# Kernel tuning notes

Measured on AMD Instinct MI355X. Metric: run time of the kernel, lower is better.

The kernel has to match this reference:

```python
import jax, jax.numpy as jnp
import numpy as np

B, S, D, H, R, P = 4, 8192, 512, 8, 64, 4
HD = D // H  # 64
EPS = 1e-6


def _sketch_p4(z, G1, G2):
    # sketchwithnegativity(z, 2): M1 = M2 = z
    inv_sqrt_r = 1.0 / np.sqrt(R).astype(np.float32)
    half = inv_sqrt_r * ((z @ G1) * (z @ G2))  # [B,H,S,R]
    return half * half  # sketch(): half * half for p=4


def setup_inputs() -> dict:
    key = jax.random.key(0)
    ks = jax.random.split(key, 16)
    lin = lambda k: jax.random.normal(k, (D, D), jnp.float32) * (1.0 / np.sqrt(D))
    g = lambda k: jax.random.normal(k, (HD, R), jnp.float32) * (1.0 / np.sqrt(R))
    return {
        "x": jax.random.normal(ks[0], (B, S, D), jnp.float32),
        "Wq": lin(ks[1]), "bq": jnp.zeros((D,), jnp.float32),
        "Wk": lin(ks[2]), "bk": jnp.zeros((D,), jnp.float32),
        "Wv": lin(ks[3]), "bv": jnp.zeros((D,), jnp.float32),
        "Wp": lin(ks[4]), "bp": jnp.zeros((D,), jnp.float32),
        "gamma_q": jnp.ones((1,), jnp.float32), "beta_q": jnp.zeros((1,), jnp.float32),
        "gamma_k": jnp.ones((1,), jnp.float32), "beta_k": jnp.zeros((1,), jnp.float32),
        "qG1": g(ks[5]), "qG2": g(ks[6]),
        "kG1": g(ks[7]), "kG2": g(ks[8]),
    }


def reference(x, Wq, bq, Wk, bk, Wv, bv, Wp, bp,
              gamma_q, beta_q, gamma_k, beta_k, qG1, qG2, kG1, kG2):
    b, s, d = x.shape
    split = lambda t: t.reshape(b, s, H, HD).transpose(0, 2, 1, 3)  # [B,H,S,HD]
    q = split(x @ Wq + bq)
    k = split(x @ Wk + bk)
    v = split(x @ Wv + bv)
    q = gamma_q * q + beta_q
    k = gamma_k * k + beta_k
    phi_q = _sketch_p4(q, qG1, qG2)  # [B,H,S,R]
    phi_k = _sketch_p4(k, kG1, kG2)  # [B,H,S,R]
    # linear-attention form of attn = (phi_q phi_k^T) / rowsum; avoids [S,S]
    kv = jnp.einsum('bhsr,bhsd->bhrd', phi_k, v)          # [B,H,R,HD]
    ksum = phi_k.sum(axis=2)                              # [B,H,R]
    num = jnp.einsum('bhqr,bhrd->bhqd', phi_q, kv)        # [B,H,S,HD]
    den = jnp.einsum('bhqr,bhr->bhq', phi_q, ksum) + EPS  # [B,H,S]
    out = num / den[..., None]
    out = out.transpose(0, 2, 1, 3).reshape(b, s, d)
    return out @ Wp + bp
```

## Files before the change

kernel.cpp:

```cpp
#include <hip/hip_runtime.h>
#include <hip/hip_bf16.h>


#define SEQ 8192

typedef __attribute__((ext_vector_type(8))) short bf16x8;
typedef __attribute__((ext_vector_type(4))) float f32x4;

__device__ __forceinline__ unsigned short f2b(float f) {
    union { float f; unsigned int i; } v; v.f = f;
    unsigned int r = v.i + 0x7fffu + ((v.i >> 16) & 1u);
    return (unsigned short)(r >> 16);
}
__device__ __forceinline__ float b2f(unsigned short u) {
    union { unsigned int i; float f; } v; v.i = ((unsigned int)u) << 16; return v.f;
}

#if __has_builtin(__builtin_amdgcn_global_load_lds)
#define ASYNC_CP 1
#endif

__device__ __forceinline__ void cp16(const unsigned short* g, unsigned short* l) {
#ifdef ASYNC_CP
    __builtin_amdgcn_global_load_lds(
        (const __attribute__((address_space(1))) unsigned int*)g,
        (__attribute__((address_space(3))) unsigned int*)l, 16, 0, 0);
#endif
}

__global__ __launch_bounds__(256) void convert_x(
    const float* __restrict__ x, unsigned short* __restrict__ xb)
{
    size_t i = ((size_t)blockIdx.x * 256 + threadIdx.x) * 8;
    float4 a = *(const float4*)&x[i];
    float4 b = *(const float4*)&x[i + 4];
    ushort4 o1 = { f2b(a.x), f2b(a.y), f2b(a.z), f2b(a.w) };
    ushort4 o2 = { f2b(b.x), f2b(b.y), f2b(b.z), f2b(b.w) };
    *(ushort4*)&xb[i]     = o1;
    *(ushort4*)&xb[i + 4] = o2;
}

__global__ __launch_bounds__(256) void convert_wT(
    const float* __restrict__ Wv, const float* __restrict__ Wp,
    unsigned short* __restrict__ WTf, unsigned short* __restrict__ WTp)
{
    const int z = blockIdx.z;
    const float* W = (z == 0) ? Wv : Wp;
    unsigned short* O = (z == 0) ? (WTf + (size_t)2048 * 512) : WTp;
    __shared__ float t[32][33];
    const int tid = threadIdx.x;
    const int tx = tid & 31, ty = tid >> 5;
    const int k0 = blockIdx.x * 32, n0 = blockIdx.y * 32;
    #pragma unroll
    for (int i = 0; i < 4; ++i)
        t[ty + 8 * i][tx] = W[(size_t)(k0 + ty + 8 * i) * 512 + n0 + tx];
    __syncthreads();
    #pragma unroll
    for (int i = 0; i < 4; ++i)
        O[(size_t)(n0 + ty + 8 * i) * 512 + k0 + tx] = f2b(t[tx][ty + 8 * i]);
}

__global__ __launch_bounds__(256) void precompute_wc(
    const float* __restrict__ Wq, const float* __restrict__ bq,
    const float* __restrict__ Wk, const float* __restrict__ bk,
    const float* __restrict__ bv,
    const float* __restrict__ gq, const float* __restrict__ bbq,
    const float* __restrict__ gk, const float* __restrict__ bbk,
    const float* __restrict__ qG1, const float* __restrict__ qG2,
    const float* __restrict__ kG1, const float* __restrict__ kG2,
    unsigned short* __restrict__ WTf, float* __restrict__ cvec)
{
    const int bi = blockIdx.x;
    const int tid = threadIdx.x;
    if (bi == 32) {
        if (blockIdx.y == 0)
            for (int i = tid; i < 512; i += 256) cvec[2048 + i] = bv[i];
        return;
    }
    const int zz = bi >> 4, h = (bi >> 1) & 7, p = bi & 1;
    const float* W    = zz ? Wk : Wq;
    const float* bias = zz ? bk : bq;
    const float* G    = zz ? (p ? kG2 : kG1) : (p ? qG2 : qG1);
    const float  gamma = zz ? gk[0] : gq[0];
    const float  beta  = zz ? bbk[0] : bbq[0];

    __shared__ float Gs[64][65];
    for (int i = tid; i < 4096; i += 256) Gs[i >> 6][i & 63] = G[i];
    __syncthreads();

    const int rr = tid & 63, kg = tid >> 6;
    const int jc = zz * 1024 + h * 128 + rr * 2 + p;
    const int k0 = blockIdx.y * 32;
    for (int k = k0 + kg; k < k0 + 32; k += 4) {
        float s = 0.f;
        const float* wrow = &W[(size_t)k * 512 + h * 64];
        #pragma unroll 8
        for (int j = 0; j < 64; ++j) s = fmaf(wrow[j], Gs[j][rr], s);
        WTf[(size_t)jc * 512 + k] = f2b(gamma * s);
    }
    if (kg == 0 && blockIdx.y == 0) {
        float cb = 0.f, cg = 0.f;
        #pragma unroll 8
        for (int j = 0; j < 64; ++j) {
            cb = fmaf(bias[h * 64 + j], Gs[j][rr], cb);
            cg += Gs[j][rr];
        }
        cvec[jc] = gamma * cb + beta * cg;
    }
}

__global__ __launch_bounds__(256) void gemm_mfma_fused(
    const unsigned short* __restrict__ xb,
    const unsigned short* __restrict__ WTf,
    const float* __restrict__ cvec,
    unsigned short* __restrict__ PHIQ, unsigned short* __restrict__ PHIKT,
    unsigned short* __restrict__ VT)
{
    __shared__ __align__(16) unsigned short As[128 * 32];
    __shared__ __align__(16) unsigned short Bs[128 * 32];
    __shared__ __align__(16) unsigned short ep[9216];

    const int tid = threadIdx.x;
    const int w = tid >> 6, lane = tid & 63;
    const int n0 = blockIdx.x * 128;
    const int j0 = blockIdx.y * 128;
    const int wr = w >> 1, wc = w & 1;

    const int r0 = w * 32 + (lane >> 2);
    const int kq = (((lane & 3) ^ ((lane >> 2) & 3)) * 8);
    const unsigned short* gA = &xb[(size_t)(n0 + r0) * 512 + kq];
    const unsigned short* gB = &WTf[(size_t)(j0 + r0) * 512 + kq];
    unsigned short* lA = &As[(w * 32) * 32];
    unsigned short* lB = &Bs[(w * 32) * 32];

    f32x4 acc[4][4];
    #pragma unroll
    for (int i = 0; i < 4; ++i)
        #pragma unroll
        for (int j = 0; j < 4; ++j) { acc[i][j] = (f32x4){0.f, 0.f, 0.f, 0.f}; }

    const int cr = (((lane >> 4) ^ (lane & 3)) * 8);

    for (int k0 = 0; k0 < 512; k0 += 32) {
        __syncthreads();
#ifdef ASYNC_CP
        cp16(gA + k0, lA);
        cp16(gA + 16 * 512 + k0, lA + 16 * 32);
        cp16(gB + k0, lB);
        cp16(gB + 16 * 512 + k0, lB + 16 * 32);
#else
        { uint4 v = *(const uint4*)(gA + k0);            *(uint4*)(lA + (size_t)lane * 8) = v; }
        { uint4 v = *(const uint4*)(gA + 16 * 512 + k0); *(uint4*)(lA + 16 * 32 + (size_t)lane * 8) = v; }
        { uint4 v = *(const uint4*)(gB + k0);            *(uint4*)(lB + (size_t)lane * 8) = v; }
        { uint4 v = *(const uint4*)(gB + 16 * 512 + k0); *(uint4*)(lB + 16 * 32 + (size_t)lane * 8) = v; }
#endif
        __syncthreads();

        bf16x8 af[4], bfr[4];
        #pragma unroll
        for (int i = 0; i < 4; ++i) {
            af[i]  = *(const bf16x8*)&As[(wr * 64 + i * 16 + (lane & 15)) * 32 + cr];
            bfr[i] = *(const bf16x8*)&Bs[(wc * 64 + i * 16 + (lane & 15)) * 32 + cr];
        }
        #pragma unroll
        for (int mi = 0; mi < 4; ++mi)
            #pragma unroll
            for (int ni = 0; ni < 4; ++ni)
                acc[mi][ni] = __builtin_amdgcn_mfma_f32_16x16x32_bf16(
                    af[mi], bfr[ni], acc[mi][ni], 0, 0, 0);
    }

    const int bq = n0 >> 13;
    const int sq = n0 & (SEQ - 1);

    if (j0 < 1024) {
        const int h = j0 >> 7;
        #pragma unroll
        for (int ni = 0; ni < 4; ++ni) {
            const int loc = wc * 64 + ni * 16 + (lane & 15);
            const float cv = cvec[j0 + loc];
            const int rr = loc >> 1;
            #pragma unroll
            for (int mi = 0; mi < 4; ++mi)
                #pragma unroll
                for (int r = 0; r < 4; ++r) {
                    float u = acc[mi][ni][r] + cv;
                    float up = __shfl_xor(u, 1);
                    float hh = 0.125f * u * up;
                    float phi = hh * hh;
                    if ((lane & 1) == 0)
                        ep[(wr * 64 + mi * 16 + (lane >> 4) * 4 + r) * 72 + rr] = f2b(phi);
                }
        }
        __syncthreads();
        for (int i = tid; i < 1024; i += 256) {
            const int tok = i >> 3, ch = i & 7;
            *(uint4*)&PHIQ[((size_t)(bq * 8 + h) * SEQ + sq + tok) * 64 + ch * 8] =
                *(const uint4*)&ep[tok * 72 + ch * 8];
        }
    } else if (j0 < 2048) {
        const int h = (j0 >> 7) & 7;
        #pragma unroll
        for (int ni = 0; ni < 4; ++ni) {
            const int loc = wc * 64 + ni * 16 + (lane & 15);
            const float cv = cvec[j0 + loc];
            const int rr = loc >> 1;
            #pragma unroll
            for (int mi = 0; mi < 4; ++mi)
                #pragma unroll
                for (int r = 0; r < 4; ++r) {
                    float u = acc[mi][ni][r] + cv;
                    float up = __shfl_xor(u, 1);
                    float hh = 0.125f * u * up;
                    float phi = hh * hh;
                    if ((lane & 1) == 0)
                        ep[rr * 136 + wr * 64 + mi * 16 + (lane >> 4) * 4 + r] = f2b(phi);
                }
        }
        __syncthreads();
        for (int i = tid; i < 1024; i += 256) {
            const int row = i >> 4, ch = i & 15;
            *(uint4*)&PHIKT[((size_t)((bq * 8 + h) * 64 + row)) * SEQ + sq + ch * 8] =
                *(const uint4*)&ep[row * 136 + ch * 8];
        }
    } else {
        #pragma unroll
        for (int half = 0; half < 2; ++half) {
            if (wc == half) {
                #pragma unroll
                for (int ni = 0; ni < 4; ++ni) {
                    const int loc = ni * 16 + (lane & 15);
                    const float cv = cvec[j0 + half * 64 + loc];
                    #pragma unroll
                    for (int mi = 0; mi < 4; ++mi)
                        #pragma unroll
                        for (int r = 0; r < 4; ++r)
                            ep[loc * 136 + wr * 64 + mi * 16 + (lane >> 4) * 4 + r] =
                                f2b(acc[mi][ni][r] + cv);
                }
            }
            __syncthreads();
            for (int i = tid; i < 1024; i += 256) {
                const int row = i >> 4, ch = i & 15;
                const int n = (j0 - 2048) + half * 64 + row;
                *(uint4*)&VT[((size_t)(bq * 512 + n)) * SEQ + sq + ch * 8] =
                    *(const uint4*)&ep[row * 136 + ch * 8];
            }
            __syncthreads();
        }
    }
}

__global__ __launch_bounds__(256) void gemm_mfma_final(
    const unsigned short* __restrict__ Ab,
    const unsigned short* __restrict__ WTp,
    const float* __restrict__ bias, float* __restrict__ out)
{
    __shared__ __align__(16) unsigned short As[128 * 32];
    __shared__ __align__(16) unsigned short Bs[128 * 32];

    const int tid = threadIdx.x;
    const int w = tid >> 6, lane = tid & 63;
    const int n0 = blockIdx.x * 128;
    const int j0 = blockIdx.y * 128;
    const int wr = w >> 1, wc = w & 1;

    const int r0 = w * 32 + (lane >> 2);
    const int kq = (((lane & 3) ^ ((lane >> 2) & 3)) * 8);
    const unsigned short* gA = &Ab[(size_t)(n0 + r0) * 512 + kq];
    const unsigned short* gB = &WTp[(size_t)(j0 + r0) * 512 + kq];
    unsigned short* lA = &As[(w * 32) * 32];
    unsigned short* lB = &Bs[(w * 32) * 32];

    f32x4 acc[4][4];
    #pragma unroll
    for (int i = 0; i < 4; ++i)
        #pragma unroll
        for (int j = 0; j < 4; ++j) { acc[i][j] = (f32x4){0.f, 0.f, 0.f, 0.f}; }

    const int cr = (((lane >> 4) ^ (lane & 3)) * 8);

    for (int k0 = 0; k0 < 512; k0 += 32) {
        __syncthreads();
#ifdef ASYNC_CP
        cp16(gA + k0, lA);
        cp16(gA + 16 * 512 + k0, lA + 16 * 32);
        cp16(gB + k0, lB);
        cp16(gB + 16 * 512 + k0, lB + 16 * 32);
#else
        { uint4 v = *(const uint4*)(gA + k0);            *(uint4*)(lA + (size_t)lane * 8) = v; }
        { uint4 v = *(const uint4*)(gA + 16 * 512 + k0); *(uint4*)(lA + 16 * 32 + (size_t)lane * 8) = v; }
        { uint4 v = *(const uint4*)(gB + k0);            *(uint4*)(lB + (size_t)lane * 8) = v; }
        { uint4 v = *(const uint4*)(gB + 16 * 512 + k0); *(uint4*)(lB + 16 * 32 + (size_t)lane * 8) = v; }
#endif
        __syncthreads();

        bf16x8 af[4], bfr[4];
        #pragma unroll
        for (int i = 0; i < 4; ++i) {
            af[i]  = *(const bf16x8*)&As[(wr * 64 + i * 16 + (lane & 15)) * 32 + cr];
            bfr[i] = *(const bf16x8*)&Bs[(wc * 64 + i * 16 + (lane & 15)) * 32 + cr];
        }
        #pragma unroll
        for (int mi = 0; mi < 4; ++mi)
            #pragma unroll
            for (int ni = 0; ni < 4; ++ni)
                acc[mi][ni] = __builtin_amdgcn_mfma_f32_16x16x32_bf16(
                    af[mi], bfr[ni], acc[mi][ni], 0, 0, 0);
    }

    #pragma unroll
    for (int ni = 0; ni < 4; ++ni) {
        const int jcol = j0 + wc * 64 + ni * 16 + (lane & 15);
        const float bvv = bias[jcol];
        #pragma unroll
        for (int mi = 0; mi < 4; ++mi) {
            #pragma unroll
            for (int r = 0; r < 4; ++r) {
                const int t = n0 + wr * 64 + mi * 16 + (lane >> 4) * 4 + r;
                out[(size_t)t * 512 + jcol] = acc[mi][ni][r] + bvv;
            }
        }
    }
}

__global__ __launch_bounds__(256) void kv_mfma(
    const unsigned short* __restrict__ PHIKT, const unsigned short* __restrict__ VT,
    float* __restrict__ KVP, float* __restrict__ KSP)
{
    const int bh = blockIdx.x, seg = blockIdx.y;
    const int tid = threadIdx.x;
    const int w = tid >> 6, lane = tid & 63;
    const size_t pbase =
        ((size_t)bh * 64 + w * 16 + (lane & 15)) * SEQ + seg * 256 + (lane >> 4) * 8;
    const size_t vbase =
        ((size_t)((bh >> 3) * 512 + (bh & 7) * 64 + (lane & 15))) * SEQ
        + seg * 256 + (lane >> 4) * 8;

    f32x4 acc[4], ks;
    #pragma unroll
    for (int nt = 0; nt < 4; ++nt) acc[nt] = (f32x4){0.f, 0.f, 0.f, 0.f};
    ks = (f32x4){0.f, 0.f, 0.f, 0.f};
    bf16x8 ones;
    #pragma unroll
    for (int i = 0; i < 8; ++i) ones[i] = (short)0x3f80;

    #pragma unroll 2
    for (int k = 0; k < 256; k += 32) {
        bf16x8 a = *(const bf16x8*)&PHIKT[pbase + k];
        ks = __builtin_amdgcn_mfma_f32_16x16x32_bf16(a, ones, ks, 0, 0, 0);
        #pragma unroll
        for (int nt = 0; nt < 4; ++nt) {
            bf16x8 bb = *(const bf16x8*)&VT[vbase + (size_t)nt * 16 * SEQ + k];
            acc[nt] = __builtin_amdgcn_mfma_f32_16x16x32_bf16(a, bb, acc[nt], 0, 0, 0);
        }
    }

    float* kvp = &KVP[((size_t)bh * 32 + seg) * 4096];
    #pragma unroll
    for (int nt = 0; nt < 4; ++nt) {
        float4 o = { acc[nt][0], acc[nt][1], acc[nt][2], acc[nt][3] };
        *(float4*)&kvp[(nt * 16 + (lane & 15)) * 64 + w * 16 + (lane >> 4) * 4] = o;
    }
    if ((lane & 15) == 0) {
        float4 o = { ks[0], ks[1], ks[2], ks[3] };
        *(float4*)&KSP[((size_t)bh * 32 + seg) * 64 + w * 16 + (lane >> 4) * 4] = o;
    }
}

__global__ __launch_bounds__(256) void kv_reduce(
    const float* __restrict__ KVP, const float* __restrict__ KSP,
    float* __restrict__ KV, float* __restrict__ KS)
{
    const int bh = blockIdx.x;
    const int e0 = blockIdx.y * 512;
    for (int e = e0 + threadIdx.x; e < e0 + 512; e += 256) {
        float s = 0.f;
        #pragma unroll 8
        for (int c = 0; c < 32; ++c) s += KVP[(size_t)(bh * 32 + c) * 4096 + e];
        KV[(size_t)bh * 4096 + e] = s;
    }
    if (blockIdx.y == 0 && threadIdx.x < 64) {
        float s = 0.f;
        for (int c = 0; c < 32; ++c) s += KSP[(bh * 32 + c) * 64 + threadIdx.x];
        KS[bh * 64 + threadIdx.x] = s;
    }
}

__global__ __launch_bounds__(256) void attn_mfma(
    const unsigned short* __restrict__ PHIQ, const float* __restrict__ KV,
    const float* __restrict__ KS, unsigned short* __restrict__ OAb)
{
    __shared__ __align__(16) unsigned short bpad[144 * 72];
    const int bh = blockIdx.x, st = blockIdx.y;
    const int tid = threadIdx.x;
    const int b = bh >> 3, h = bh & 7;

    for (int i = tid; i < 144 * 64; i += 256) {
        const int n = i >> 6, r = i & 63;
        float val;
        if (n < 64)        val = KV[(size_t)bh * 4096 + n * 64 + r];
        else if (n < 128)  { float x = KV[(size_t)bh * 4096 + (n - 64) * 64 + r];
                             val = x - b2f(f2b(x)); }
        else if (n == 128) val = KS[bh * 64 + r];
        else if (n == 129) { float x = KS[bh * 64 + r]; val = x - b2f(f2b(x)); }
        else               val = 0.f;
        bpad[n * 72 + r] = f2b(val);
    }
    __syncthreads();

    const int w = tid >> 6, lane = tid & 63;
    bf16x8 bf[9][2];
    #pragma unroll
    for (int nt = 0; nt < 9; ++nt) {
        const unsigned short* bp = &bpad[(nt * 16 + (lane & 15)) * 72 + (lane >> 4) * 8];
        bf[nt][0] = *(const bf16x8*)bp;
        bf[nt][1] = *(const bf16x8*)(bp + 32);
    }

    const int tw = st * 256 + w * 64;
    #pragma unroll
    for (int mt = 0; mt < 4; ++mt) {
        const unsigned short* ap =
            &PHIQ[((size_t)bh * SEQ + tw + mt * 16 + (lane & 15)) * 64 + (lane >> 4) * 8];
        bf16x8 a0 = *(const bf16x8*)ap;
        bf16x8 a1 = *(const bf16x8*)(ap + 32);
        f32x4 acc[9];
        #pragma unroll
        for (int nt = 0; nt < 9; ++nt) acc[nt] = (f32x4){0.f, 0.f, 0.f, 0.f};
        #pragma unroll
        for (int nt = 0; nt < 9; ++nt) {
            acc[nt] = __builtin_amdgcn_mfma_f32_16x16x32_bf16(a0, bf[nt][0], acc[nt], 0, 0, 0);
            acc[nt] = __builtin_amdgcn_mfma_f32_16x16x32_bf16(a1, bf[nt][1], acc[nt], 0, 0, 0);
        }
        #pragma unroll
        for (int r4 = 0; r4 < 4; ++r4) {
            const float den = __shfl(acc[8][r4], (lane & 48)) +
                              __shfl(acc[8][r4], (lane & 48) + 1) + 1e-6f;
            const float inv = 1.0f / den;
            const int s = tw + mt * 16 + (lane >> 4) * 4 + r4;
            #pragma unroll
            for (int nt = 0; nt < 4; ++nt)
                OAb[((size_t)b * SEQ + s) * 512 + h * 64 + nt * 16 + (lane & 15)] =
                    f2b((acc[nt][r4] + acc[nt + 4][r4]) * inv);
        }
    }
}

extern "C" void kernel_launch(void* const* d_in, const int* in_sizes, int n_in,
                              void* d_out, int out_size, void* d_ws, size_t ws_size,
                              hipStream_t stream)
{
    (void)in_sizes; (void)n_in; (void)out_size; (void)ws_size;
    const float* x   = (const float*)d_in[0];
    const float* Wq  = (const float*)d_in[1];
    const float* bq  = (const float*)d_in[2];
    const float* Wk  = (const float*)d_in[3];
    const float* bk  = (const float*)d_in[4];
    const float* Wv  = (const float*)d_in[5];
    const float* bv  = (const float*)d_in[6];
    const float* Wp  = (const float*)d_in[7];
    const float* bp  = (const float*)d_in[8];
    const float* gq  = (const float*)d_in[9];
    const float* bbq = (const float*)d_in[10];
    const float* gk  = (const float*)d_in[11];
    const float* bbk = (const float*)d_in[12];
    const float* qG1 = (const float*)d_in[13];
    const float* qG2 = (const float*)d_in[14];
    const float* kG1 = (const float*)d_in[15];
    const float* kG2 = (const float*)d_in[16];

    unsigned short* PHIQ  = (unsigned short*)d_ws;
    unsigned short* PHIKT = PHIQ + 16777216;
    unsigned short* VT    = PHIKT + 16777216;
    unsigned short* xb    = VT   + 16777216;
    unsigned short* OAb   = xb   + 16777216;
    unsigned short* WTf   = OAb  + 16777216;
    unsigned short* WTp   = WTf  + 2560 * 512;
    float* cvec = (float*)(WTp + 262144);
    float* KVP  = cvec + 2560;
    float* KSP  = KVP + 4194304;
    float* KV   = KSP + 65536;
    float* KS   = KV + 131072;
    float* out  = (float*)d_out;

    hipLaunchKernelGGL(convert_x, dim3(8192), dim3(256), 0, stream, x, xb);
    hipLaunchKernelGGL(convert_wT, dim3(16, 16, 2), dim3(256), 0, stream,
                       Wv, Wp, WTf, WTp);
    hipLaunchKernelGGL(precompute_wc, dim3(33, 16), dim3(256), 0, stream,
                       Wq, bq, Wk, bk, bv, gq, bbq, gk, bbk,
                       qG1, qG2, kG1, kG2, WTf, cvec);
    hipLaunchKernelGGL(gemm_mfma_fused, dim3(256, 20), dim3(256), 0, stream,
                       xb, WTf, cvec, PHIQ, PHIKT, VT);
    hipLaunchKernelGGL(kv_mfma, dim3(32, 32), dim3(256), 0, stream,
                       PHIKT, VT, KVP, KSP);
    hipLaunchKernelGGL(kv_reduce, dim3(32, 8), dim3(256), 0, stream, KVP, KSP, KV, KS);
    hipLaunchKernelGGL(attn_mfma, dim3(32, 32), dim3(256), 0, stream,
                       PHIQ, KV, KS, OAb);
    hipLaunchKernelGGL(gemm_mfma_final, dim3(256, 4), dim3(256), 0, stream,
                       OAb, WTp, bp, out);
}
```

Before: 417.0 us.

## Merge prep kernels, swap GEMM grid order, alias LDS, drop swizzle, halve KV segments

Folds the three preprocessing kernels into one prep_all launch that dispatches on block index, removing two launches. The two GEMM kernels swap grid axes so blocks sharing an x row tile launch next to each other, which should improve L2 reuse of the A operand. The fused GEMM aliases the epilogue buffer onto the A/B staging LDS to cut shared memory per block, guarded by an added barrier. The XOR swizzle on LDS loads is removed, which may reintroduce bank conflicts. kv_mfma now processes 512-length segments with 16 partials instead of 32, halving partial writes and reduce work but also halving parallelism.

```diff
diff --git a/kernel.cpp b/kernel.cpp
--- a/kernel.cpp
+++ b/kernel.cpp
@@ -28,39 +28,10 @@
 #endif
 }
 
-__global__ __launch_bounds__(256) void convert_x(
-    const float* __restrict__ x, unsigned short* __restrict__ xb)
-{
-    size_t i = ((size_t)blockIdx.x * 256 + threadIdx.x) * 8;
-    float4 a = *(const float4*)&x[i];
-    float4 b = *(const float4*)&x[i + 4];
-    ushort4 o1 = { f2b(a.x), f2b(a.y), f2b(a.z), f2b(a.w) };
-    ushort4 o2 = { f2b(b.x), f2b(b.y), f2b(b.z), f2b(b.w) };
-    *(ushort4*)&xb[i]     = o1;
-    *(ushort4*)&xb[i + 4] = o2;
-}
-
-__global__ __launch_bounds__(256) void convert_wT(
+__global__ __launch_bounds__(256) void prep_all(
+    const float* __restrict__ x, unsigned short* __restrict__ xb,
     const float* __restrict__ Wv, const float* __restrict__ Wp,
-    unsigned short* __restrict__ WTf, unsigned short* __restrict__ WTp)
-{
-    const int z = blockIdx.z;
-    const float* W = (z == 0) ? Wv : Wp;
-    unsigned short* O = (z == 0) ? (WTf + (size_t)2048 * 512) : WTp;
-    __shared__ float t[32][33];
-    const int tid = threadIdx.x;
-    const int tx = tid & 31, ty = tid >> 5;
-    const int k0 = blockIdx.x * 32, n0 = blockIdx.y * 32;
-    #pragma unroll
-    for (int i = 0; i < 4; ++i)
-        t[ty + 8 * i][tx] = W[(size_t)(k0 + ty + 8 * i) * 512 + n0 + tx];
-    __syncthreads();
-    #pragma unroll
-    for (int i = 0; i < 4; ++i)
-        O[(size_t)(n0 + ty + 8 * i) * 512 + k0 + tx] = f2b(t[tx][ty + 8 * i]);
-}
-
-__global__ __launch_bounds__(256) void precompute_wc(
+    unsigned short* __restrict__ WTf, unsigned short* __restrict__ WTp,
     const float* __restrict__ Wq, const float* __restrict__ bq,
     const float* __restrict__ Wk, const float* __restrict__ bk,
     const float* __restrict__ bv,
@@ -68,15 +39,46 @@
     const float* __restrict__ gk, const float* __restrict__ bbk,
     const float* __restrict__ qG1, const float* __restrict__ qG2,
     const float* __restrict__ kG1, const float* __restrict__ kG2,
-    unsigned short* __restrict__ WTf, float* __restrict__ cvec)
-{
-    const int bi = blockIdx.x;
+    float* __restrict__ cvec)
+{
+    const int blk = blockIdx.x;
     const int tid = threadIdx.x;
-    if (bi == 32) {
-        if (blockIdx.y == 0)
-            for (int i = tid; i < 512; i += 256) cvec[2048 + i] = bv[i];
+
+    if (blk < 8192) {
+        size_t i = ((size_t)blk * 256 + tid) * 8;
+        float4 a = *(const float4*)&x[i];
+        float4 b = *(const float4*)&x[i + 4];
+        ushort4 o1 = { f2b(a.x), f2b(a.y), f2b(a.z), f2b(a.w) };
+        ushort4 o2 = { f2b(b.x), f2b(b.y), f2b(b.z), f2b(b.w) };
+        *(ushort4*)&xb[i]     = o1;
+        *(ushort4*)&xb[i + 4] = o2;
         return;
     }
+
+    if (blk < 8704) {
+        const int idx = blk - 8192;
+        const int z = idx >> 8;
+        const float* W = (z == 0) ? Wv : Wp;
+        unsigned short* O = (z == 0) ? (WTf + (size_t)2048 * 512) : WTp;
+        __shared__ float t[32][33];
+        const int tx = tid & 31, ty = tid >> 5;
+        const int k0 = ((idx >> 4) & 15) * 32, n0 = (idx & 15) * 32;
+        #pragma unroll
+        for (int i = 0; i < 4; ++i)
+            t[ty + 8 * i][tx] = W[(size_t)(k0 + ty + 8 * i) * 512 + n0 + tx];
+        __syncthreads();
+        #pragma unroll
+        for (int i = 0; i < 4; ++i)
+            O[(size_t)(n0 + ty + 8 * i) * 512 + k0 + tx] = f2b(t[tx][ty + 8 * i]);
+        return;
+    }
+
+    const int idx = blk - 8704;
+    if (idx == 512) {
+        for (int i = tid; i < 512; i += 256) cvec[2048 + i] = bv[i];
+        return;
+    }
+    const int bi = idx & 31, ky = idx >> 5;
     const int zz = bi >> 4, h = (bi >> 1) & 7, p = bi & 1;
     const float* W    = zz ? Wk : Wq;
     const float* bias = zz ? bk : bq;
@@ -90,7 +92,7 @@
 
     const int rr = tid & 63, kg = tid >> 6;
     const int jc = zz * 1024 + h * 128 + rr * 2 + p;
-    const int k0 = blockIdx.y * 32;
+    const int k0 = ky * 32;
     for (int k = k0 + kg; k < k0 + 32; k += 4) {
         float s = 0.f;
         const float* wrow = &W[(size_t)k * 512 + h * 64];
@@ -98,7 +100,7 @@
         for (int j = 0; j < 64; ++j) s = fmaf(wrow[j], Gs[j][rr], s);
         WTf[(size_t)jc * 512 + k] = f2b(gamma * s);
     }
-    if (kg == 0 && blockIdx.y == 0) {
+    if (kg == 0 && ky == 0) {
         float cb = 0.f, cg = 0.f;
         #pragma unroll 8
         for (int j = 0; j < 64; ++j) {
@@ -116,22 +118,23 @@
     unsigned short* __restrict__ PHIQ, unsigned short* __restrict__ PHIKT,
     unsigned short* __restrict__ VT)
 {
-    __shared__ __align__(16) unsigned short As[128 * 32];
-    __shared__ __align__(16) unsigned short Bs[128 * 32];
-    __shared__ __align__(16) unsigned short ep[9216];
+    __shared__ __align__(16) unsigned short smem[9216];
+    unsigned short* As = smem;
+    unsigned short* Bs = smem + 4096;
+    unsigned short* ep = smem;
 
     const int tid = threadIdx.x;
     const int w = tid >> 6, lane = tid & 63;
-    const int n0 = blockIdx.x * 128;
-    const int j0 = blockIdx.y * 128;
+    const int j0 = blockIdx.x * 128;
+    const int n0 = blockIdx.y * 128;
     const int wr = w >> 1, wc = w & 1;
 
     const int r0 = w * 32 + (lane >> 2);
-    const int kq = (((lane & 3) ^ ((lane >> 2) & 3)) * 8);
+    const int kq = (lane & 3) * 8;
     const unsigned short* gA = &xb[(size_t)(n0 + r0) * 512 + kq];
     const unsigned short* gB = &WTf[(size_t)(j0 + r0) * 512 + kq];
-    unsigned short* lA = &As[(w * 32) * 32];
-    unsigned short* lB = &Bs[(w * 32) * 32];
+    unsigned short* lA = As + (w * 32) * 32;
+    unsigned short* lB = Bs + (w * 32) * 32;
 
     f32x4 acc[4][4];
     #pragma unroll
@@ -139,7 +142,7 @@
         #pragma unroll
         for (int j = 0; j < 4; ++j) { acc[i][j] = (f32x4){0.f, 0.f, 0.f, 0.f}; }
 
-    const int cr = (((lane >> 4) ^ (lane & 3)) * 8);
+    const int cr = (lane >> 4) * 8;
 
     for (int k0 = 0; k0 < 512; k0 += 32) {
         __syncthreads();
@@ -170,6 +173,7 @@
                     af[mi], bfr[ni], acc[mi][ni], 0, 0, 0);
     }
 
+    __syncthreads();
     const int bq = n0 >> 13;
     const int sq = n0 & (SEQ - 1);
 
@@ -261,12 +265,12 @@
 
     const int tid = threadIdx.x;
     const int w = tid >> 6, lane = tid & 63;
-    const int n0 = blockIdx.x * 128;
-    const int j0 = blockIdx.y * 128;
+    const int j0 = blockIdx.x * 128;
+    const int n0 = blockIdx.y * 128;
     const int wr = w >> 1, wc = w & 1;
 
     const int r0 = w * 32 + (lane >> 2);
-    const int kq = (((lane & 3) ^ ((lane >> 2) & 3)) * 8);
+    const int kq = (lane & 3) * 8;
     const unsigned short* gA = &Ab[(size_t)(n0 + r0) * 512 + kq];
     const unsigned short* gB = &WTp[(size_t)(j0 + r0) * 512 + kq];
     unsigned short* lA = &As[(w * 32) * 32];
@@ -278,7 +282,7 @@
         #pragma unroll
         for (int j = 0; j < 4; ++j) { acc[i][j] = (f32x4){0.f, 0.f, 0.f, 0.f}; }
 
-    const int cr = (((lane >> 4) ^ (lane & 3)) * 8);
+    const int cr = (lane >> 4) * 8;
 
     for (int k0 = 0; k0 < 512; k0 += 32) {
         __syncthreads();
@@ -332,10 +336,10 @@
     const int tid = threadIdx.x;
     const int w = tid >> 6, lane = tid & 63;
     const size_t pbase =
-        ((size_t)bh * 64 + w * 16 + (lane & 15)) * SEQ + seg * 256 + (lane >> 4) * 8;
+        ((size_t)bh * 64 + w * 16 + (lane & 15)) * SEQ + seg * 512 + (lane >> 4) * 8;
     const size_t vbase =
         ((size_t)((bh >> 3) * 512 + (bh & 7) * 64 + (lane & 15))) * SEQ
-        + seg * 256 + (lane >> 4) * 8;
+        + seg * 512 + (lane >> 4) * 8;
 
     f32x4 acc[4], ks;
     #pragma unroll
@@ -346,7 +350,7 @@
     for (int i = 0; i < 8; ++i) ones[i] = (short)0x3f80;
 
     #pragma unroll 2
-    for (int k = 0; k < 256; k += 32) {
+    for (int k = 0; k < 512; k += 32) {
         bf16x8 a = *(const bf16x8*)&PHIKT[pbase + k];
         ks = __builtin_amdgcn_mfma_f32_16x16x32_bf16(a, ones, ks, 0, 0, 0);
         #pragma unroll
@@ -356,7 +360,7 @@
         }
     }
 
-    float* kvp = &KVP[((size_t)bh * 32 + seg) * 4096];
+    float* kvp = &KVP[((size_t)bh * 16 + seg) * 4096];
     #pragma unroll
     for (int nt = 0; nt < 4; ++nt) {
         float4 o = { acc[nt][0], acc[nt][1], acc[nt][2], acc[nt][3] };
@@ -364,7 +368,7 @@
     }
     if ((lane & 15) == 0) {
         float4 o = { ks[0], ks[1], ks[2], ks[3] };
-        *(float4*)&KSP[((size_t)bh * 32 + seg) * 64 + w * 16 + (lane >> 4) * 4] = o;
+        *(float4*)&KSP[((size_t)bh * 16 + seg) * 64 + w * 16 + (lane >> 4) * 4] = o;
     }
 }
 
@@ -377,12 +381,12 @@
     for (int e = e0 + threadIdx.x; e < e0 + 512; e += 256) {
         float s = 0.f;
         #pragma unroll 8
-        for (int c = 0; c < 32; ++c) s += KVP[(size_t)(bh * 32 + c) * 4096 + e];
+        for (int c = 0; c < 16; ++c) s += KVP[(size_t)(bh * 16 + c) * 4096 + e];
         KV[(size_t)bh * 4096 + e] = s;
     }
     if (blockIdx.y == 0 && threadIdx.x < 64) {
         float s = 0.f;
-        for (int c = 0; c < 32; ++c) s += KSP[(bh * 32 + c) * 64 + threadIdx.x];
+        for (int c = 0; c < 16; ++c) s += KSP[(bh * 16 + c) * 64 + threadIdx.x];
         KS[bh * 64 + threadIdx.x] = s;
     }
 }
@@ -484,19 +488,17 @@
     float* KS   = KV + 131072;
     float* out  = (float*)d_out;
 
-    hipLaunchKernelGGL(convert_x, dim3(8192), dim3(256), 0, stream, x, xb);
-    hipLaunchKernelGGL(convert_wT, dim3(16, 16, 2), dim3(256), 0, stream,
-                       Wv, Wp, WTf, WTp);
-    hipLaunchKernelGGL(precompute_wc, dim3(33, 16), dim3(256), 0, stream,
+    hipLaunchKernelGGL(prep_all, dim3(9217), dim3(256), 0, stream,
+                       x, xb, Wv, Wp, WTf, WTp,
                        Wq, bq, Wk, bk, bv, gq, bbq, gk, bbk,
-                       qG1, qG2, kG1, kG2, WTf, cvec);
-    hipLaunchKernelGGL(gemm_mfma_fused, dim3(256, 20), dim3(256), 0, stream,
+                       qG1, qG2, kG1, kG2, cvec);
+    hipLaunchKernelGGL(gemm_mfma_fused, dim3(20, 256), dim3(256), 0, stream,
                        xb, WTf, cvec, PHIQ, PHIKT, VT);
-    hipLaunchKernelGGL(kv_mfma, dim3(32, 32), dim3(256), 0, stream,
+    hipLaunchKernelGGL(kv_mfma, dim3(32, 16), dim3(256), 0, stream,
                        PHIKT, VT, KVP, KSP);
     hipLaunchKernelGGL(kv_reduce, dim3(32, 8), dim3(256), 0, stream, KVP, KSP, KV, KS);
     hipLaunchKernelGGL(attn_mfma, dim3(32, 32), dim3(256), 0, stream,
                        PHIQ, KV, KS, OAb);
-    hipLaunchKernelGGL(gemm_mfma_final, dim3(256, 4), dim3(256), 0, stream,
+    hipLaunchKernelGGL(gemm_mfma_final, dim3(4, 256), dim3(256), 0, stream,
                        OAb, WTp, bp, out);
 }
```

Result: slower. 432.3 us (+3.7%).
